# Performance work log

Hardware: AMD Instinct MI355X
Metric: run time of the kernel (lower is better)

## Reference

```python
import jax, jax.numpy as jnp
import numpy as np

BN_EPS = 1e-5


def setup_inputs() -> dict:
    key = jax.random.key(0)
    ks = jax.random.split(key, 12)
    B, C, N = 8, 256, 2048
    s = 1.0 / np.sqrt(C)
    x = jax.random.normal(ks[0], (B, C, N), dtype=jnp.float32)
    gamma = jnp.ones((C,), jnp.float32)
    beta = jnp.zeros((C,), jnp.float32)
    Wq = jax.random.normal(ks[1], (C, C), jnp.float32) * s
    bq = jnp.zeros((C,), jnp.float32)
    Wk = jax.random.normal(ks[2], (C, C), jnp.float32) * s
    bk = jnp.zeros((C,), jnp.float32)
    Wv = jax.random.normal(ks[3], (C, C), jnp.float32) * s
    bv = jnp.zeros((C,), jnp.float32)
    Wp = jax.random.normal(ks[4], (C, C), jnp.float32) * s
    bp = jnp.zeros((C,), jnp.float32)
    return {"x": x, "gamma": gamma, "beta": beta, "Wq": Wq, "bq": bq,
            "Wk": Wk, "bk": bk, "Wv": Wv, "bv": bv, "Wp": Wp, "bp": bp}


def reference(x, gamma, beta, Wq, bq, Wk, bk, Wv, bv, Wp, bp):
    B, C, N = x.shape
    # BatchNorm1d (training-mode batch stats): normalize per channel over (B, N)
    mean = jnp.mean(x, axis=(0, 2), keepdims=True)            # [1,C,1]
    var = jnp.mean(jnp.square(x - mean), axis=(0, 2), keepdims=True)
    h = (x - mean) * jax.lax.rsqrt(var + BN_EPS)
    h = h * gamma[None, :, None] + beta[None, :, None]
    # 1x1 Conv1d projections == per-position channel GEMMs
    q = jnp.einsum('oc,bcn->bno', Wq, h) + bq[None, None, :]  # [B,N,C]
    k = jnp.einsum('oc,bcn->bon', Wk, h) + bk[None, :, None]  # [B,C,N]
    v = jnp.einsum('oc,bcn->bno', Wv, h) + bv[None, None, :]  # [B,N,C]
    scale = jnp.asarray(C, x.dtype) ** -0.5
    w = jnp.einsum('bnc,bcm->bnm', q, k) * scale              # [B,N,N]
    w = jax.nn.softmax(w, axis=-1)
    h = jnp.einsum('bnm,bmc->bnc', w, v)                      # [B,N,C]
    out = jnp.einsum('oc,bnc->bon', Wp, h) + bp[None, :, None]  # [B,C,N]
    return x + out
```

## Files before the change

### kernel.cpp

```cpp
#include <hip/hip_runtime.h>
#include <hip/hip_fp16.h>

typedef _Float16 f16x8 __attribute__((ext_vector_type(8)));
typedef _Float16 f16x4 __attribute__((ext_vector_type(4)));
typedef float f32x4 __attribute__((ext_vector_type(4)));
typedef float f32x16 __attribute__((ext_vector_type(16)));

#define MFMA16(a, b, c) __builtin_amdgcn_mfma_f32_16x16x32_f16(a, b, c, 0, 0, 0)
#define MFMA32(a, b, c) __builtin_amdgcn_mfma_f32_32x32x16_f16(a, b, c, 0, 0, 0)

__device__ __forceinline__ void gload_lds16(const _Float16* g, void* l) {
    __builtin_amdgcn_global_load_lds(
        (const __attribute__((address_space(1))) void*)g,
        (__attribute__((address_space(3))) void*)l, 16, 0, 0);
}

__device__ __forceinline__ unsigned pkh(float a, float b) {
    typedef __fp16 fp16v2 __attribute__((ext_vector_type(2)));
    fp16v2 h = __builtin_amdgcn_cvt_pkrtz(a, b);
    return __builtin_bit_cast(unsigned, h);
}

__device__ __forceinline__ float fexp2(float x) {
#if __has_builtin(__builtin_amdgcn_exp2f)
    return __builtin_amdgcn_exp2f(x);
#else
    return exp2f(x);
#endif
}

__global__ __launch_bounds__(256) void trans_stats_kernel(
    const float* __restrict__ x, _Float16* __restrict__ xt,
    float* __restrict__ sums)
{
    __shared__ float tile[64][65];
    int t = threadIdx.x;
    int b = blockIdx.z, c0 = blockIdx.y * 64, n0 = blockIdx.x * 64;
    int nl = t & 63, cq = t >> 6;
#pragma unroll
    for (int r = 0; r < 16; ++r) {
        int cl = cq * 16 + r;
        tile[cl][nl] = x[((size_t)b * 256 + c0 + cl) * 2048 + n0 + nl];
    }
    __syncthreads();
    int cl2 = t & 63, nq = t >> 6;
#pragma unroll
    for (int r = 0; r < 16; ++r) {
        int nl2 = nq * 16 + r;
        xt[((size_t)b * 2048 + n0 + nl2) * 256 + c0 + cl2] = (_Float16)tile[nl2 & 63 ? cl2 : cl2][nl2];
    }
    if (t < 64) {
        float s = 0.f, ss = 0.f;
#pragma unroll
        for (int j = 0; j < 64; ++j) {
            float v = tile[t][j];
            s += v; ss += v * v;
        }
        atomicAdd(&sums[c0 + t], s);
        atomicAdd(&sums[256 + c0 + t], ss);
    }
}

__global__ __launch_bounds__(256) void fold_kernel(
    const float* __restrict__ Wq, const float* __restrict__ Wk,
    const float* __restrict__ Wv, const float* __restrict__ Wp,
    const float* __restrict__ bq, const float* __restrict__ bk,
    const float* __restrict__ bv,
    const float* __restrict__ gamma, const float* __restrict__ beta,
    const float* __restrict__ sums,
    _Float16* __restrict__ wbf, float* __restrict__ bfold)
{
    int t = threadIdx.x, bid = blockIdx.x;
    if (bid >= 192) {
        int i = (bid - 192) * 256 + t;
        wbf[3 * 65536 + i] = (_Float16)Wp[i];
        return;
    }
    __shared__ float sc[256], sh[256];
    if (t < 256) {
        float mean = sums[t] * (1.f / 16384.f);
        float var  = sums[256 + t] * (1.f / 16384.f) - mean * mean;
        float rstd = rsqrtf(var + 1e-5f);
        float s = rstd * gamma[t];
        sc[t] = s;
        sh[t] = beta[t] - mean * s;
    }
    __syncthreads();
    const float QS = 0.09016844005556021f;
    int mat = bid >> 6;
    int o = (bid & 63) * 4 + (t >> 6);
    int lane = t & 63;
    const float* W  = (mat == 0) ? Wq : (mat == 1) ? Wk : Wv;
    const float* bb = (mat == 0) ? bq : (mat == 1) ? bk : bv;
    float qs = (mat == 0) ? QS : 1.f;
    float dot = 0.f;
    _Float16* wd = wbf + mat * 65536 + o * 256;
#pragma unroll
    for (int i = 0; i < 4; ++i) {
        int c = lane * 4 + i;
        float wv_ = W[o * 256 + c];
        dot += wv_ * sh[c];
        wd[c] = (_Float16)(wv_ * sc[c] * qs);
    }
#pragma unroll
    for (int off = 32; off > 0; off >>= 1) dot += __shfl_down(dot, off, 64);
    if (lane == 0) bfold[mat * 256 + o] = qs * (bb[o] + dot);
}

template<int BN, int WGM, int WGN, typename OT, bool BIAS_I, bool RES>
__global__ __launch_bounds__(256, 3) void gemm_nt(
    const _Float16* __restrict__ Aall, long strideA,
    const _Float16* __restrict__ Ball, long strideB,
    const float* __restrict__ bias,
    const float* __restrict__ resid, long strideR,
    OT* __restrict__ Call, long strideC, int Nn)
{
    constexpr int BM = 128;
    constexpr int WR = BM / WGM;
    constexpr int WC = BN / WGN;
    constexpr int FM = WR / 16, FN = WC / 16;
    constexpr int BUFSZ = 8192 + BN * 64;
    constexpr int NI = 8 + BN / 16;
    constexpr int PW = NI / 4;

    int b = blockIdx.z;
    const _Float16* A  = Aall + (size_t)b * strideA;
    const _Float16* Bm = Ball + (size_t)b * strideB;
    OT* C = Call + (size_t)b * strideC;
    int i0 = blockIdx.y * BM, j0 = blockIdx.x * BN;

    __shared__ __align__(16) char lds[2 * BUFSZ];

    int t = threadIdx.x, lane = t & 63, w = t >> 6;
    int lr = lane & 15, lg = lane >> 4;
    int wm = w % WGM, wn = w / WGM;

    int soff = (lane >> 2) * 256 + (((lane & 3) ^ ((lane >> 3) & 3))) * 8;
    int lgx16 = ((lg ^ ((lr >> 1) & 3))) * 16;

    f32x4 acc[FM][FN] = {};

    auto stage = [&](int kk, int buf) {
#pragma unroll
        for (int i = 0; i < PW; ++i) {
            int u = w * PW + i;
            if (u < 8)
                gload_lds16(A + (size_t)(i0 + u * 16) * 256 + kk * 32 + soff,
                            lds + buf * BUFSZ + u * 1024);
            else
                gload_lds16(Bm + (size_t)(j0 + (u - 8) * 16) * 256 + kk * 32 + soff,
                            lds + buf * BUFSZ + 8192 + (u - 8) * 1024);
        }
    };

    stage(0, 0);
    __syncthreads();
    int buf = 0;
#pragma unroll
    for (int kk = 0; kk < 8; ++kk) {
        if (kk + 1 < 8) stage(kk + 1, buf ^ 1);
        const char* ab = lds + buf * BUFSZ;
        const char* bb = ab + 8192;
        f16x8 af[FM], bf[FN];
#pragma unroll
        for (int f = 0; f < FM; ++f)
            af[f] = *(const f16x8*)(ab + (wm * WR + f * 16 + lr) * 64 + lgx16);
#pragma unroll
        for (int f = 0; f < FN; ++f)
            bf[f] = *(const f16x8*)(bb + (wn * WC + f * 16 + lr) * 64 + lgx16);
        __builtin_amdgcn_s_setprio(1);
#pragma unroll
        for (int fm = 0; fm < FM; ++fm)
#pragma unroll
            for (int fn = 0; fn < FN; ++fn)
                acc[fm][fn] = MFMA16(af[fm], bf[fn], acc[fm][fn]);
        __builtin_amdgcn_s_setprio(0);
        __syncthreads();
        buf ^= 1;
    }
#pragma unroll
    for (int fm = 0; fm < FM; ++fm)
#pragma unroll
        for (int fn = 0; fn < FN; ++fn)
#pragma unroll
            for (int rr = 0; rr < 4; ++rr) {
                int row = i0 + wm * WR + fm * 16 + lg * 4 + rr;
                int col = j0 + wn * WC + fn * 16 + lr;
                float vv = acc[fm][fn][rr] + (BIAS_I ? bias[row] : bias[col]);
                if (RES) vv += resid[(size_t)b * strideR + (size_t)row * Nn + col];
                C[(size_t)row * Nn + col] = (OT)vv;
            }
}

__global__ __launch_bounds__(256, 2) void attn7_kernel(
    const _Float16* __restrict__ qk, const _Float16* __restrict__ vb,
    _Float16* __restrict__ Opart, float* __restrict__ lpart,
    int nsp, int mspan)
{
    int id = blockIdx.x;
    int b = id & 7;
    int rest = id >> 3;
    int qblk = rest & 15, sp = rest >> 4;
    int m_base = sp * mspan;
    int T = mspan >> 5;

    __shared__ __align__(16) char lds[66560];

    int t = threadIdx.x, ln = t & 63, w = t >> 6;
    int col = ln & 31, hi = ln >> 5;

    const _Float16* kg = qk + (size_t)b * 1048576 + 256;
    const _Float16* vg = vb + (size_t)b * 524288;

    int koffs[4], voffs[4];
#pragma unroll
    for (int i = 0; i < 4; ++i) {
        int n = w * 4 + i;
        koffs[i] = (ln >> 1) * 512 + (ln & 1) * 8 + n * 16;
        voffs[i] = (((n & 7) * 32 + (ln >> 1)) * 2048) + ((n >> 3) * 16) + (ln & 1) * 8;
    }
    int frd = col * 32 + hi * 16;

    f16x8 qf[16];
    {
        const _Float16* qp = qk + ((size_t)b * 2048 + qblk * 128 + w * 32 + col) * 512 + hi * 8;
#pragma unroll
        for (int ks = 0; ks < 16; ++ks) qf[ks] = *(const f16x8*)(qp + ks * 16);
    }

    f32x16 oacc[8] = {};
    float l_run = 0.f;
    unsigned W[8];

#pragma unroll
    for (int i = 0; i < 4; ++i) {
        gload_lds16(kg + (size_t)(m_base) * 512 + koffs[i], lds + (w * 4 + i) * 1024);
        gload_lds16(vg + m_base + voffs[i], lds + 16384 + (w * 4 + i) * 1024);
        gload_lds16(kg + (size_t)(m_base + 32) * 512 + koffs[i], lds + 32768 + (w * 4 + i) * 1024);
        gload_lds16(vg + m_base + 32 + voffs[i], lds + 49152 + (w * 4 + i) * 1024);
    }
    asm volatile("s_waitcnt vmcnt(0)" ::: "memory");
    __builtin_amdgcn_sched_barrier(0);
    __builtin_amdgcn_s_barrier();
    {
        f32x16 sn = {};
        __builtin_amdgcn_s_setprio(1);
#pragma unroll
        for (int ks = 0; ks < 16; ++ks) {
            f16x8 kf = *(const f16x8*)(lds + ks * 1024 + frd);
            sn = MFMA32(kf, qf[ks], sn);
        }
        __builtin_amdgcn_s_setprio(0);
        float pv_[16];
#pragma unroll
        for (int i = 0; i < 16; ++i) pv_[i] = fexp2(sn[i] - 16.f);
        float psum = ((pv_[0]+pv_[1]) + (pv_[2]+pv_[3])) + ((pv_[4]+pv_[5]) + (pv_[6]+pv_[7]))
                   + ((pv_[8]+pv_[9]) + (pv_[10]+pv_[11])) + ((pv_[12]+pv_[13]) + (pv_[14]+pv_[15]));
        psum += __shfl_xor(psum, 32, 64);
        l_run = psum;
        W[0] = pkh(pv_[0],  pv_[1]);  W[1] = pkh(pv_[2],  pv_[3]);
        W[2] = pkh(pv_[4],  pv_[5]);  W[3] = pkh(pv_[6],  pv_[7]);
        W[4] = pkh(pv_[8],  pv_[9]);  W[5] = pkh(pv_[10], pv_[11]);
        W[6] = pkh(pv_[12], pv_[13]); W[7] = pkh(pv_[14], pv_[15]);
    }
    __builtin_amdgcn_s_barrier();

    for (int tt = 0; tt < T - 1; ++tt) {
        char* myb = lds + (tt & 1) * 32768;
        char* nxb = lds + ((tt + 1) & 1) * 32768;
        if (tt + 2 < T) {
            int m0 = m_base + (tt + 2) * 32;
#pragma unroll
            for (int i = 0; i < 4; ++i)
                gload_lds16(kg + (size_t)m0 * 512 + koffs[i], myb + (w * 4 + i) * 1024);
        }
        union { unsigned u[4]; f16x8 v; } pf0, pf1;
        {
            unsigned sx0 = hi ? W[0] : W[2], sx1 = hi ? W[1] : W[3];
            unsigned r0 = __shfl_xor(sx0, 32, 64), r1 = __shfl_xor(sx1, 32, 64);
            pf0.u[0] = hi ? r0 : W[0]; pf0.u[1] = hi ? r1 : W[1];
            pf0.u[2] = hi ? W[2] : r0; pf0.u[3] = hi ? W[3] : r1;
        }
        {
            unsigned sx0 = hi ? W[4] : W[6], sx1 = hi ? W[5] : W[7];
            unsigned r0 = __shfl_xor(sx0, 32, 64), r1 = __shfl_xor(sx1, 32, 64);
            pf1.u[0] = hi ? r0 : W[4]; pf1.u[1] = hi ? r1 : W[5];
            pf1.u[2] = hi ? W[6] : r0; pf1.u[3] = hi ? W[7] : r1;
        }
        f32x16 sn = {};
        __builtin_amdgcn_s_setprio(1);
#pragma unroll
        for (int g = 0; g < 4; ++g) {
#pragma unroll
            for (int k2 = 0; k2 < 4; ++k2) {
                int ks = g * 4 + k2;
                f16x8 kf = *(const f16x8*)(nxb + ks * 1024 + frd);
                sn = MFMA32(kf, qf[ks], sn);
            }
#pragma unroll
            for (int k2 = 0; k2 < 4; ++k2) {
                int idx = g * 4 + k2;
                f16x8 vf = *(const f16x8*)(myb + 16384 + idx * 1024 + frd);
                oacc[idx & 7] = MFMA32(vf, (g < 2) ? pf0.v : pf1.v, oacc[idx & 7]);
            }
        }
        __builtin_amdgcn_s_setprio(0);
        {
            float pv_[16];
#pragma unroll
            for (int i = 0; i < 16; ++i) pv_[i] = fexp2(sn[i] - 16.f);
            float psum = ((pv_[0]+pv_[1]) + (pv_[2]+pv_[3])) + ((pv_[4]+pv_[5]) + (pv_[6]+pv_[7]))
                       + ((pv_[8]+pv_[9]) + (pv_[10]+pv_[11])) + ((pv_[12]+pv_[13]) + (pv_[14]+pv_[15]));
            psum += __shfl_xor(psum, 32, 64);
            l_run += psum;
            W[0] = pkh(pv_[0],  pv_[1]);  W[1] = pkh(pv_[2],  pv_[3]);
            W[2] = pkh(pv_[4],  pv_[5]);  W[3] = pkh(pv_[6],  pv_[7]);
            W[4] = pkh(pv_[8],  pv_[9]);  W[5] = pkh(pv_[10], pv_[11]);
            W[6] = pkh(pv_[12], pv_[13]); W[7] = pkh(pv_[14], pv_[15]);
        }
        __builtin_amdgcn_s_barrier();
        __builtin_amdgcn_sched_barrier(0);
        if (tt + 2 < T) {
            int m0 = m_base + (tt + 2) * 32;
#pragma unroll
            for (int i = 0; i < 4; ++i)
                gload_lds16(vg + m0 + voffs[i], myb + 16384 + (w * 4 + i) * 1024);
        }
        asm volatile("s_waitcnt vmcnt(4)" ::: "memory");
        __builtin_amdgcn_sched_barrier(0);
        __builtin_amdgcn_s_barrier();
    }

    asm volatile("s_waitcnt vmcnt(0)" ::: "memory");
    __builtin_amdgcn_sched_barrier(0);
    __builtin_amdgcn_s_barrier();
    {
        char* myb = lds + ((T - 1) & 1) * 32768;
        union { unsigned u[4]; f16x8 v; } pf0, pf1;
        {
            unsigned sx0 = hi ? W[0] : W[2], sx1 = hi ? W[1] : W[3];
            unsigned r0 = __shfl_xor(sx0, 32, 64), r1 = __shfl_xor(sx1, 32, 64);
            pf0.u[0] = hi ? r0 : W[0]; pf0.u[1] = hi ? r1 : W[1];
            pf0.u[2] = hi ? W[2] : r0; pf0.u[3] = hi ? W[3] : r1;
        }
        {
            unsigned sx0 = hi ? W[4] : W[6], sx1 = hi ? W[5] : W[7];
            unsigned r0 = __shfl_xor(sx0, 32, 64), r1 = __shfl_xor(sx1, 32, 64);
            pf1.u[0] = hi ? r0 : W[4]; pf1.u[1] = hi ? r1 : W[5];
            pf1.u[2] = hi ? W[6] : r0; pf1.u[3] = hi ? W[7] : r1;
        }
        __builtin_amdgcn_s_setprio(1);
#pragma unroll
        for (int idx = 0; idx < 16; ++idx) {
            f16x8 vf = *(const f16x8*)(myb + 16384 + idx * 1024 + frd);
            oacc[idx & 7] = MFMA32(vf, (idx < 8) ? pf0.v : pf1.v, oacc[idx & 7]);
        }
        __builtin_amdgcn_s_setprio(0);
    }
    __builtin_amdgcn_s_barrier();

    _Float16* tr = (_Float16*)(lds + w * 16640);
    float invl = 1.0f / l_run;
#pragma unroll
    for (int dt = 0; dt < 8; ++dt)
#pragma unroll
        for (int g = 0; g < 4; ++g) {
            f16x4 q4;
#pragma unroll
            for (int e = 0; e < 4; ++e) q4[e] = (_Float16)(oacc[dt][g * 4 + e] * invl);
            int d0 = dt * 32 + g * 8 + 4 * hi;
            *(f16x4*)(tr + col * 260 + d0) = q4;
        }
    size_t region = ((size_t)((sp * 8 + b) * 16 + qblk)) * 32768;
    int rrow = ln >> 1, h = ln & 1;
    const _Float16* srcr = tr + rrow * 260 + h * 128;
    _Float16* dstr = Opart + region + (size_t)(w * 32 + rrow) * 256 + h * 128;
#pragma unroll
    for (int i = 0; i < 16; ++i)
        *(f16x8*)(dstr + i * 8) = *(const f16x8*)(srcr + i * 8);

    if (hi == 0) {
        int qi = w * 32 + col;
        lpart[((sp * 8 + b) * 16 + qblk) * 128 + qi] = l_run;
    }
}

__global__ __launch_bounds__(256) void combine3_kernel(
    const _Float16* __restrict__ Opart, const float* __restrict__ lpart,
    _Float16* __restrict__ abuf, int nsp)
{
    int id = blockIdx.x;
    int b = id & 7, qb = (id >> 3) & 15, dh = id >> 7;
    int t = threadIdx.x;
    __shared__ float cf[4][128];
    if (t < 128) {
        float l[4], s = 0.f;
        for (int sp = 0; sp < nsp; ++sp) {
            l[sp] = lpart[((sp * 8 + b) * 16 + qb) * 128 + t];
            s += l[sp];
        }
        float inv = 1.0f / s;
        for (int sp = 0; sp < nsp; ++sp) cf[sp][t] = l[sp] * inv;
    }
    __syncthreads();
    size_t rb = ((size_t)(b * 16 + qb)) * 32768;
#pragma unroll
    for (int i = 0; i < 8; ++i) {
        int flat = i * 2048 + t * 8;
        int qi = flat >> 7, dl = flat & 127;
        float acc[8] = {};
        for (int sp = 0; sp < nsp; ++sp) {
            f16x8 v = *(const f16x8*)(Opart + (size_t)sp * 4194304 + rb +
                                      (size_t)qi * 256 + dh * 128 + dl);
            float c = cf[sp][qi];
#pragma unroll
            for (int e = 0; e < 8; ++e) acc[e] += c * (float)v[e];
        }
        f16x8 r;
#pragma unroll
        for (int e = 0; e < 8; ++e) r[e] = (_Float16)acc[e];
        *(f16x8*)(abuf + ((size_t)b * 2048 + qb * 128 + qi) * 256 + dh * 128 + dl) = r;
    }
}

extern "C" void kernel_launch(void* const* d_in, const int* in_sizes, int n_in,
                              void* d_out, int out_size, void* d_ws, size_t ws_size,
                              hipStream_t stream) {
    const float* x     = (const float*)d_in[0];
    const float* gamma = (const float*)d_in[1];
    const float* beta  = (const float*)d_in[2];
    const float* Wq    = (const float*)d_in[3];
    const float* bq    = (const float*)d_in[4];
    const float* Wk    = (const float*)d_in[5];
    const float* bk    = (const float*)d_in[6];
    const float* Wv    = (const float*)d_in[7];
    const float* bv    = (const float*)d_in[8];
    const float* Wp    = (const float*)d_in[9];
    const float* bp    = (const float*)d_in[10];
    float* out = (float*)d_out;

    char* ws = (char*)d_ws;
    float* sums  = (float*)ws;
    float* bfold = (float*)(ws + 2048);
    float* lpart = (float*)(ws + 8192);
    _Float16* wbf   = (_Float16*)(ws + 524288);
    _Float16* xt    = (_Float16*)(ws + 1048576);
    _Float16* qkbuf = (_Float16*)(ws + 9437184);
    _Float16* vbuf  = (_Float16*)(ws + 26214400);
    _Float16* Opart = (_Float16*)(ws + 34603008);
    _Float16* abuf  = xt;

    int nsp = (ws_size >= (size_t)34603008 + 4ull * 8388608ull) ? 4 : 2;
    int mspan = 2048 / nsp;

    const long SB = 524288;

    hipMemsetAsync(sums, 0, 2048, stream);
    trans_stats_kernel<<<dim3(32, 4, 8), 256, 0, stream>>>(x, xt, sums);
    fold_kernel<<<448, 256, 0, stream>>>(Wq, Wk, Wv, Wp, bq, bk, bv,
                                         gamma, beta, sums, wbf, bfold);
    gemm_nt<128, 2, 2, _Float16, false, false><<<dim3(4, 16, 8), 256, 0, stream>>>(
        xt, SB, wbf, 0, bfold, nullptr, 0, qkbuf, 1048576, 512);
    gemm_nt<64, 4, 1, _Float16, true, false><<<dim3(32, 2, 8), 256, 0, stream>>>(
        wbf + 131072, 0, xt, SB, bfold + 512, nullptr, 0, vbuf, SB, 2048);
    attn7_kernel<<<128 * nsp, 256, 0, stream>>>(qkbuf, vbuf, Opart, lpart,
                                                nsp, mspan);
    combine3_kernel<<<256, 256, 0, stream>>>(Opart, lpart, abuf, nsp);
    gemm_nt<64, 4, 1, float, true, true><<<dim3(32, 2, 8), 256, 0, stream>>>(
        wbf + 196608, 0, abuf, SB, bp, x, SB, out, SB, 2048);
}
```

Before: 110.9 us.

## Write K and V directly in MFMA fragment order so attention loads are contiguous

The projection GEMMs get new epilogue modes that store K and V pre-swizzled into the per-lane fragment layout the attention kernel reads. The attention kernel can then fill shared memory with fully contiguous 1 KB chunks instead of strided gathers. The fused Q/K GEMM is split into three separate GEMMs (Q, K-fragment, V-fragment), which adds a launch and changes the tile shape in exchange for simpler, coalesced attention loads. The epilogue stores 8-byte chunks scattered by fragment index, which may coalesce less well on the write side.

```diff
diff --git a/kernel.cpp b/kernel.cpp
--- a/kernel.cpp
+++ b/kernel.cpp
@@ -47,7 +47,7 @@
 #pragma unroll
     for (int r = 0; r < 16; ++r) {
         int nl2 = nq * 16 + r;
-        xt[((size_t)b * 2048 + n0 + nl2) * 256 + c0 + cl2] = (_Float16)tile[nl2 & 63 ? cl2 : cl2][nl2];
+        xt[((size_t)b * 2048 + n0 + nl2) * 256 + c0 + cl2] = (_Float16)tile[cl2][nl2];
     }
     if (t < 64) {
         float s = 0.f, ss = 0.f;
@@ -107,7 +107,7 @@
     if (lane == 0) bfold[mat * 256 + o] = qs * (bb[o] + dot);
 }
 
-template<int BN, int WGM, int WGN, typename OT, bool BIAS_I, bool RES>
+template<int BN, int WGM, int WGN, typename OT, bool BIAS_I, bool RES, int EPI>
 __global__ __launch_bounds__(256, 3) void gemm_nt(
     const _Float16* __restrict__ Aall, long strideA,
     const _Float16* __restrict__ Ball, long strideB,
@@ -178,22 +178,52 @@
         __syncthreads();
         buf ^= 1;
     }
-#pragma unroll
-    for (int fm = 0; fm < FM; ++fm)
-#pragma unroll
-        for (int fn = 0; fn < FN; ++fn)
-#pragma unroll
-            for (int rr = 0; rr < 4; ++rr) {
-                int row = i0 + wm * WR + fm * 16 + lg * 4 + rr;
-                int col = j0 + wn * WC + fn * 16 + lr;
-                float vv = acc[fm][fn][rr] + (BIAS_I ? bias[row] : bias[col]);
-                if (RES) vv += resid[(size_t)b * strideR + (size_t)row * Nn + col];
-                C[(size_t)row * Nn + col] = (OT)vv;
+    if constexpr (EPI == 0) {
+#pragma unroll
+        for (int fm = 0; fm < FM; ++fm)
+#pragma unroll
+            for (int fn = 0; fn < FN; ++fn)
+#pragma unroll
+                for (int rr = 0; rr < 4; ++rr) {
+                    int row = i0 + wm * WR + fm * 16 + lg * 4 + rr;
+                    int col = j0 + wn * WC + fn * 16 + lr;
+                    float vv = acc[fm][fn][rr] + (BIAS_I ? bias[row] : bias[col]);
+                    if (RES) vv += resid[(size_t)b * strideR + (size_t)row * Nn + col];
+                    C[(size_t)row * Nn + col] = (OT)vv;
+                }
+    } else {
+#pragma unroll
+        for (int fm = 0; fm < FM; ++fm)
+#pragma unroll
+            for (int fn = 0; fn < FN; ++fn) {
+                int row0 = i0 + wm * WR + fm * 16 + lg * 4;
+                int col  = j0 + wn * WC + fn * 16 + lr;
+                f16x4 q4;
+#pragma unroll
+                for (int rr = 0; rr < 4; ++rr) {
+                    float vv = acc[fm][fn][rr] + (BIAS_I ? bias[row0 + rr] : bias[col]);
+                    q4[rr] = (_Float16)vv;
+                }
+                size_t off;
+                if constexpr (EPI == 1) {
+                    int mt = col >> 5, mloc = col & 31;
+                    int ks = row0 >> 4;
+                    int ln2 = mloc + 32 * (lg >> 1);
+                    off = (((size_t)mt * 16 + ks) * 64 + ln2) * 8 + (lg & 1) * 4;
+                } else {
+                    int mt = row0 >> 5, ms = (row0 >> 4) & 1;
+                    int dt = col >> 5, dloc = col & 31;
+                    int ln2 = dloc + 32 * (lg >> 1);
+                    off = ((((size_t)mt * 2 + ms) * 8 + dt) * 64 + ln2) * 8 + (lg & 1) * 4;
+                }
+                *(f16x4*)((_Float16*)C + off) = q4;
             }
-}
-
-__global__ __launch_bounds__(256, 2) void attn7_kernel(
-    const _Float16* __restrict__ qk, const _Float16* __restrict__ vb,
+    }
+}
+
+__global__ __launch_bounds__(256, 2) void attn8_kernel(
+    const _Float16* __restrict__ qb, const _Float16* __restrict__ kfrag,
+    const _Float16* __restrict__ vfrag,
     _Float16* __restrict__ Opart, float* __restrict__ lpart,
     int nsp, int mspan)
 {
@@ -201,7 +231,6 @@
     int b = id & 7;
     int rest = id >> 3;
     int qblk = rest & 15, sp = rest >> 4;
-    int m_base = sp * mspan;
     int T = mspan >> 5;
 
     __shared__ __align__(16) char lds[66560];
@@ -209,21 +238,14 @@
     int t = threadIdx.x, ln = t & 63, w = t >> 6;
     int col = ln & 31, hi = ln >> 5;
 
-    const _Float16* kg = qk + (size_t)b * 1048576 + 256;
-    const _Float16* vg = vb + (size_t)b * 524288;
-
-    int koffs[4], voffs[4];
-#pragma unroll
-    for (int i = 0; i < 4; ++i) {
-        int n = w * 4 + i;
-        koffs[i] = (ln >> 1) * 512 + (ln & 1) * 8 + n * 16;
-        voffs[i] = (((n & 7) * 32 + (ln >> 1)) * 2048) + ((n >> 3) * 16) + (ln & 1) * 8;
-    }
-    int frd = col * 32 + hi * 16;
+    const _Float16* kg = kfrag + (size_t)b * 524288 + (size_t)(sp * T) * 8192 + ln * 8;
+    const _Float16* vg = vfrag + (size_t)b * 524288 + (size_t)(sp * T) * 8192 + ln * 8;
+    int c0 = w * 4;
+    int frd = ln * 16;
 
     f16x8 qf[16];
     {
-        const _Float16* qp = qk + ((size_t)b * 2048 + qblk * 128 + w * 32 + col) * 512 + hi * 8;
+        const _Float16* qp = qb + ((size_t)b * 2048 + qblk * 128 + w * 32 + col) * 256 + hi * 8;
 #pragma unroll
         for (int ks = 0; ks < 16; ++ks) qf[ks] = *(const f16x8*)(qp + ks * 16);
     }
@@ -234,10 +256,11 @@
 
 #pragma unroll
     for (int i = 0; i < 4; ++i) {
-        gload_lds16(kg + (size_t)(m_base) * 512 + koffs[i], lds + (w * 4 + i) * 1024);
-        gload_lds16(vg + m_base + voffs[i], lds + 16384 + (w * 4 + i) * 1024);
-        gload_lds16(kg + (size_t)(m_base + 32) * 512 + koffs[i], lds + 32768 + (w * 4 + i) * 1024);
-        gload_lds16(vg + m_base + 32 + voffs[i], lds + 49152 + (w * 4 + i) * 1024);
+        int c = c0 + i;
+        gload_lds16(kg + c * 512,        lds + c * 1024);
+        gload_lds16(vg + c * 512,        lds + 16384 + c * 1024);
+        gload_lds16(kg + 8192 + c * 512, lds + 32768 + c * 1024);
+        gload_lds16(vg + 8192 + c * 512, lds + 49152 + c * 1024);
     }
     asm volatile("s_waitcnt vmcnt(0)" ::: "memory");
     __builtin_amdgcn_sched_barrier(0);
@@ -269,10 +292,10 @@
         char* myb = lds + (tt & 1) * 32768;
         char* nxb = lds + ((tt + 1) & 1) * 32768;
         if (tt + 2 < T) {
-            int m0 = m_base + (tt + 2) * 32;
+            const _Float16* ks2 = kg + (size_t)(tt + 2) * 8192;
 #pragma unroll
             for (int i = 0; i < 4; ++i)
-                gload_lds16(kg + (size_t)m0 * 512 + koffs[i], myb + (w * 4 + i) * 1024);
+                gload_lds16(ks2 + (c0 + i) * 512, myb + (c0 + i) * 1024);
         }
         union { unsigned u[4]; f16x8 v; } pf0, pf1;
         {
@@ -321,10 +344,10 @@
         __builtin_amdgcn_s_barrier();
         __builtin_amdgcn_sched_barrier(0);
         if (tt + 2 < T) {
-            int m0 = m_base + (tt + 2) * 32;
+            const _Float16* vs2 = vg + (size_t)(tt + 2) * 8192;
 #pragma unroll
             for (int i = 0; i < 4; ++i)
-                gload_lds16(vg + m0 + voffs[i], myb + 16384 + (w * 4 + i) * 1024);
+                gload_lds16(vs2 + (c0 + i) * 512, myb + 16384 + (c0 + i) * 1024);
         }
         asm volatile("s_waitcnt vmcnt(4)" ::: "memory");
         __builtin_amdgcn_sched_barrier(0);
@@ -445,8 +468,9 @@
     float* lpart = (float*)(ws + 8192);
     _Float16* wbf   = (_Float16*)(ws + 524288);
     _Float16* xt    = (_Float16*)(ws + 1048576);
-    _Float16* qkbuf = (_Float16*)(ws + 9437184);
-    _Float16* vbuf  = (_Float16*)(ws + 26214400);
+    _Float16* qbuf  = (_Float16*)(ws + 9437184);
+    _Float16* kfrag = (_Float16*)(ws + 17825792);
+    _Float16* vfrag = (_Float16*)(ws + 26214400);
     _Float16* Opart = (_Float16*)(ws + 34603008);
     _Float16* abuf  = xt;
 
@@ -459,13 +483,15 @@
     trans_stats_kernel<<<dim3(32, 4, 8), 256, 0, stream>>>(x, xt, sums);
     fold_kernel<<<448, 256, 0, stream>>>(Wq, Wk, Wv, Wp, bq, bk, bv,
                                          gamma, beta, sums, wbf, bfold);
-    gemm_nt<128, 2, 2, _Float16, false, false><<<dim3(4, 16, 8), 256, 0, stream>>>(
-        xt, SB, wbf, 0, bfold, nullptr, 0, qkbuf, 1048576, 512);
-    gemm_nt<64, 4, 1, _Float16, true, false><<<dim3(32, 2, 8), 256, 0, stream>>>(
-        wbf + 131072, 0, xt, SB, bfold + 512, nullptr, 0, vbuf, SB, 2048);
-    attn7_kernel<<<128 * nsp, 256, 0, stream>>>(qkbuf, vbuf, Opart, lpart,
+    gemm_nt<64, 4, 1, _Float16, false, false, 0><<<dim3(4, 16, 8), 256, 0, stream>>>(
+        xt, SB, wbf, 0, bfold, nullptr, 0, qbuf, SB, 256);
+    gemm_nt<64, 4, 1, _Float16, true, false, 1><<<dim3(32, 2, 8), 256, 0, stream>>>(
+        wbf + 65536, 0, xt, SB, bfold + 256, nullptr, 0, kfrag, SB, 2048);
+    gemm_nt<64, 4, 1, _Float16, false, false, 2><<<dim3(4, 16, 8), 256, 0, stream>>>(
+        xt, SB, wbf + 131072, 0, bfold + 512, nullptr, 0, vfrag, SB, 256);
+    attn8_kernel<<<128 * nsp, 256, 0, stream>>>(qbuf, kfrag, vfrag, Opart, lpart,
                                                 nsp, mspan);
     combine3_kernel<<<256, 256, 0, stream>>>(Opart, lpart, abuf, nsp);
-    gemm_nt<64, 4, 1, float, true, true><<<dim3(32, 2, 8), 256, 0, stream>>>(
+    gemm_nt<64, 4, 1, float, true, true, 0><<<dim3(32, 2, 8), 256, 0, stream>>>(
         wbf + 196608, 0, abuf, SB, bp, x, SB, out, SB, 2048);
 }
```

Result: no change. 112.5 us (+1.5%).
